# Kernel tuning notes

Measured on AMD Instinct MI355X. Metric: run time of the kernel, lower is better.

Reference implementation:

```python
import jax, jax.numpy as jnp
import numpy as np


def setup_inputs() -> dict:
    key = jax.random.key(0)
    ks = jax.random.split(key, 5)
    B, Cin, Ch, H, W, K = 8, 64, 64, 128, 128, 3
    fan_in = (Cin + Ch) * K * K
    return {
        "x": jax.random.normal(ks[0], (B, Cin, H, W), jnp.float32),
        "prev_h": jax.random.normal(ks[1], (B, Ch, H, W), jnp.float32),
        "prev_c": jax.random.normal(ks[2], (B, Ch, H, W), jnp.float32),
        "W_gates": jax.random.normal(ks[3], (4 * Ch, Cin + Ch, K, K), jnp.float32) / np.sqrt(fan_in),
        "b_gates": jax.random.normal(ks[4], (4 * Ch,), jnp.float32) * 0.01,
    }


def reference(x, prev_h, prev_c, W_gates, b_gates):
    # ConvLSTM cell: conv over concat(input, prev_h) -> 4 gates -> gating.
    pad = W_gates.shape[-1] // 2
    stacked = jnp.concatenate([x, prev_h], axis=1)  # [B, Cin+Ch, H, W]
    gates = jax.lax.conv_general_dilated(
        stacked, W_gates,
        window_strides=(1, 1),
        padding=[(pad, pad), (pad, pad)],
        dimension_numbers=("NCHW", "OIHW", "NCHW"),
    ) + b_gates[None, :, None, None]  # [B, 4*Ch, H, W]
    in_gate, remember_gate, out_gate, cell_gate = jnp.split(gates, 4, axis=1)
    in_gate = jax.nn.sigmoid(in_gate)
    remember_gate = jax.nn.sigmoid(remember_gate)
    out_gate = jax.nn.sigmoid(out_gate)
    cell_gate = jnp.tanh(cell_gate)
    cell = in_gate * cell_gate + remember_gate * prev_c
    hidden = out_gate * jnp.tanh(cell)
    return (hidden, cell)
```

## Files before the change

### kernel.cpp

```cpp
#include <hip/hip_runtime.h>

typedef __attribute__((ext_vector_type(8))) short short8;
typedef __attribute__((ext_vector_type(4))) short short4v;
typedef __attribute__((ext_vector_type(4))) float float4v;

#define NPIX_HID 8388608
#define PST 132

__device__ __forceinline__ short f2bf(float f) {
    union { float f; unsigned u; } v; v.f = f;
    unsigned r = (v.u + 0x7FFFu + ((v.u >> 16) & 1u)) >> 16;
    return (short)r;
}

__device__ __forceinline__ float sigmoidf_(float v) { return 1.f / (1.f + __expf(-v)); }
__device__ __forceinline__ float tanhf_(float v)    { return 2.f / (1.f + __expf(-2.f * v)) - 1.f; }

__global__ void wprep(const float* __restrict__ W, short* __restrict__ A) {
    int tid = blockIdx.x * 256 + threadIdx.x;
    if (tid >= 9 * 16 * 256 * 8) return;
    int j   = tid & 7;
    int co  = (tid >> 3) & 255;
    int cig = (tid >> 11) & 15;
    int kk  = tid >> 15;
    int ci  = cig * 8 + j;
    A[tid] = f2bf(W[co * 1152 + ci * 9 + kk]);
}

__global__ __launch_bounds__(256, 2) void convlstm_main(
    const float* __restrict__ x, const float* __restrict__ ph,
    const float* __restrict__ pc, const short* __restrict__ aprep,
    const float* __restrict__ bg, float* __restrict__ out)
{
    __shared__ short Bs[4 * 66 * PST];

    const int tid  = threadIdx.x;
    const int lane = tid & 63;
    const int wave = tid >> 6;
    const int l15  = lane & 15;
    const int quad = lane >> 4;

    const int t  = blockIdx.x;
    const int x0 = (t & 1) * 64;
    const int y0 = ((t >> 1) & 63) * 2;
    const int b  = t >> 7;

    for (int i = tid; i < 4224; i += 256) {
        const int px  = i % 66;
        const int ro  = i / 66;
        const int oct = ro & 15;
        const int row = ro >> 4;
        const int ysrc = y0 + row - 1;
        const int xsrc = x0 + px - 1;
        short4v lo = {0,0,0,0}, hi = {0,0,0,0};
        if ((unsigned)ysrc < 128u && (unsigned)xsrc < 128u) {
            const float* src = (oct < 8) ? x : ph;
            const float* sp = src + (((b * 64 + (oct & 7) * 8) * 128 + ysrc) * 128 + xsrc);
#pragma unroll
            for (int j = 0; j < 4; ++j) lo[j] = f2bf(sp[j * 16384]);
#pragma unroll
            for (int j = 0; j < 4; ++j) hi[j] = f2bf(sp[(j + 4) * 16384]);
        }
        short* dst = &Bs[(row * 66 + px) * PST + oct * 8];
        *(short4v*)dst       = lo;
        *(short4v*)(dst + 4) = hi;
    }
    __syncthreads();

    float4v acc[4][8];
#pragma unroll
    for (int mt = 0; mt < 4; ++mt)
#pragma unroll
        for (int nt = 0; nt < 8; ++nt)
            acc[mt][nt] = (float4v){0.f, 0.f, 0.f, 0.f};

    const short* ap = aprep + quad * 2048 + (wave * 16 + l15) * 8;
    short8 abuf[2][4];
#pragma unroll
    for (int mt = 0; mt < 4; ++mt) abuf[0][mt] = *(const short8*)(ap + mt * 512);

    const short* bb = &Bs[l15 * PST + quad * 8];

#pragma unroll 1
    for (int ky = 0; ky < 3; ++ky) {
#pragma unroll 1
        for (int kx = 0; kx < 3; ++kx) {
#pragma unroll
            for (int kc = 0; kc < 4; ++kc) {
                const int cur = kc & 1, nxt = cur ^ 1;
                const bool last = (ky == 2) & (kx == 2) & (kc == 3);
                const short* apn = last ? ap : (ap + 8192);
#pragma unroll
                for (int mt = 0; mt < 4; ++mt)
                    abuf[nxt][mt] = *(const short8*)(apn + mt * 512);
                ap = apn;

                short8 bfr[8];
#pragma unroll
                for (int nt = 0; nt < 8; ++nt) {
                    const short* bp = bb + (nt >> 2) * (66 * PST) + (nt & 3) * (16 * PST) + kc * 32;
                    short4v lo = *(const short4v*)bp;
                    short4v hi = *(const short4v*)(bp + 4);
                    bfr[nt] = __builtin_shufflevector(lo, hi, 0, 1, 2, 3, 4, 5, 6, 7);
                }
#pragma unroll
                for (int mt = 0; mt < 4; ++mt)
#pragma unroll
                    for (int nt = 0; nt < 8; ++nt)
                        acc[mt][nt] = __builtin_amdgcn_mfma_f32_16x16x32_bf16(
                            abuf[cur][mt], bfr[nt], acc[mt][nt], 0, 0, 0);
            }
            bb += PST;
        }
        bb += 63 * PST;
    }

#pragma unroll
    for (int nt = 0; nt < 8; ++nt) {
        const int y  = y0 + (nt >> 2);
        const int px = x0 + ((nt & 3) << 4) + l15;
#pragma unroll
        for (int r = 0; r < 4; ++r) {
            const int c = wave * 16 + quad * 4 + r;
            const float gi = acc[0][nt][r] + bg[c];
            const float gf = acc[1][nt][r] + bg[64 + c];
            const float go = acc[2][nt][r] + bg[128 + c];
            const float gc = acc[3][nt][r] + bg[192 + c];
            const float ig = sigmoidf_(gi);
            const float fg = sigmoidf_(gf);
            const float og = sigmoidf_(go);
            const float cg = tanhf_(gc);
            const int idx = ((b * 64 + c) * 128 + y) * 128 + px;
            const float cell = ig * cg + fg * pc[idx];
            const float hid  = og * tanhf_(cell);
            out[idx] = hid;
            out[NPIX_HID + idx] = cell;
        }
    }
}

extern "C" void kernel_launch(void* const* d_in, const int* in_sizes, int n_in,
                              void* d_out, int out_size, void* d_ws, size_t ws_size,
                              hipStream_t stream) {
    const float* x  = (const float*)d_in[0];
    const float* ph = (const float*)d_in[1];
    const float* pc = (const float*)d_in[2];
    const float* W  = (const float*)d_in[3];
    const float* bg = (const float*)d_in[4];
    float* out = (float*)d_out;
    short* aprep = (short*)d_ws;

    wprep<<<1152, 256, 0, stream>>>(W, aprep);
    convlstm_main<<<1024, 256, 0, stream>>>(x, ph, pc, aprep, bg, out);
}
```

Baseline: 219.5 us.

## Halve output tile to one row per block and double-buffer B fragments

Each block now computes a single output row of 64 pixels instead of two rows, which halves the accumulator registers and the LDS halo tile. The launch doubles the grid and asks for three blocks per CU. B-operand fragments are also prefetched one k-chunk ahead into a double buffer, so LDS reads overlap the MFMAs. The cost is less reuse of the halo and weights per block: 3 input rows are staged per output row instead of 4 per two rows, and weight loads per output are doubled.

```diff
diff --git a/kernel.cpp b/kernel.cpp
--- a/kernel.cpp
+++ b/kernel.cpp
@@ -27,12 +27,12 @@
     A[tid] = f2bf(W[co * 1152 + ci * 9 + kk]);
 }
 
-__global__ __launch_bounds__(256, 2) void convlstm_main(
+__global__ __launch_bounds__(256, 3) void convlstm_main(
     const float* __restrict__ x, const float* __restrict__ ph,
     const float* __restrict__ pc, const short* __restrict__ aprep,
     const float* __restrict__ bg, float* __restrict__ out)
 {
-    __shared__ short Bs[4 * 66 * PST];
+    __shared__ short Bs[3 * 66 * PST];
 
     const int tid  = threadIdx.x;
     const int lane = tid & 63;
@@ -42,10 +42,10 @@
 
     const int t  = blockIdx.x;
     const int x0 = (t & 1) * 64;
-    const int y0 = ((t >> 1) & 63) * 2;
-    const int b  = t >> 7;
+    const int y0 = (t >> 1) & 127;
+    const int b  = t >> 8;
 
-    for (int i = tid; i < 4224; i += 256) {
+    for (int i = tid; i < 3168; i += 256) {
         const int px  = i % 66;
         const int ro  = i / 66;
         const int oct = ro & 15;
@@ -67,11 +67,11 @@
     }
     __syncthreads();
 
-    float4v acc[4][8];
+    float4v acc[4][4];
 #pragma unroll
     for (int mt = 0; mt < 4; ++mt)
 #pragma unroll
-        for (int nt = 0; nt < 8; ++nt)
+        for (int nt = 0; nt < 4; ++nt)
             acc[mt][nt] = (float4v){0.f, 0.f, 0.f, 0.f};
 
     const short* ap = aprep + quad * 2048 + (wave * 16 + l15) * 8;
@@ -80,45 +80,56 @@
     for (int mt = 0; mt < 4; ++mt) abuf[0][mt] = *(const short8*)(ap + mt * 512);
 
     const short* bb = &Bs[l15 * PST + quad * 8];
+    short8 bfr[2][4];
+#pragma unroll
+    for (int nt = 0; nt < 4; ++nt) {
+        const short* bp = bb + nt * (16 * PST);
+        short4v lo = *(const short4v*)bp;
+        short4v hi = *(const short4v*)(bp + 4);
+        bfr[0][nt] = __builtin_shufflevector(lo, hi, 0, 1, 2, 3, 4, 5, 6, 7);
+    }
 
 #pragma unroll 1
     for (int ky = 0; ky < 3; ++ky) {
 #pragma unroll 1
         for (int kx = 0; kx < 3; ++kx) {
+            const bool lastkx = (ky == 2) & (kx == 2);
+            const short* bbn = bb + ((kx == 2) ? 64 * PST : PST);
 #pragma unroll
             for (int kc = 0; kc < 4; ++kc) {
                 const int cur = kc & 1, nxt = cur ^ 1;
-                const bool last = (ky == 2) & (kx == 2) & (kc == 3);
+                const bool last = lastkx & (kc == 3);
+
                 const short* apn = last ? ap : (ap + 8192);
 #pragma unroll
                 for (int mt = 0; mt < 4; ++mt)
                     abuf[nxt][mt] = *(const short8*)(apn + mt * 512);
                 ap = apn;
 
-                short8 bfr[8];
+                const short* bq = (kc == 3) ? (lastkx ? bb : bbn) : bb;
+                const int kcn = (kc + 1) & 3;
 #pragma unroll
-                for (int nt = 0; nt < 8; ++nt) {
-                    const short* bp = bb + (nt >> 2) * (66 * PST) + (nt & 3) * (16 * PST) + kc * 32;
+                for (int nt = 0; nt < 4; ++nt) {
+                    const short* bp = bq + nt * (16 * PST) + kcn * 32;
                     short4v lo = *(const short4v*)bp;
                     short4v hi = *(const short4v*)(bp + 4);
-                    bfr[nt] = __builtin_shufflevector(lo, hi, 0, 1, 2, 3, 4, 5, 6, 7);
+                    bfr[nxt][nt] = __builtin_shufflevector(lo, hi, 0, 1, 2, 3, 4, 5, 6, 7);
                 }
+
 #pragma unroll
                 for (int mt = 0; mt < 4; ++mt)
 #pragma unroll
-                    for (int nt = 0; nt < 8; ++nt)
+                    for (int nt = 0; nt < 4; ++nt)
                         acc[mt][nt] = __builtin_amdgcn_mfma_f32_16x16x32_bf16(
-                            abuf[cur][mt], bfr[nt], acc[mt][nt], 0, 0, 0);
+                            abuf[cur][mt], bfr[cur][nt], acc[mt][nt], 0, 0, 0);
             }
-            bb += PST;
+            bb = bbn;
         }
-        bb += 63 * PST;
     }
 
 #pragma unroll
-    for (int nt = 0; nt < 8; ++nt) {
-        const int y  = y0 + (nt >> 2);
-        const int px = x0 + ((nt & 3) << 4) + l15;
+    for (int nt = 0; nt < 4; ++nt) {
+        const int px = x0 + (nt << 4) + l15;
 #pragma unroll
         for (int r = 0; r < 4; ++r) {
             const int c = wave * 16 + quad * 4 + r;
@@ -130,7 +141,7 @@
             const float fg = sigmoidf_(gf);
             const float og = sigmoidf_(go);
             const float cg = tanhf_(gc);
-            const int idx = ((b * 64 + c) * 128 + y) * 128 + px;
+            const int idx = ((b * 64 + c) * 128 + y0) * 128 + px;
             const float cell = ig * cg + fg * pc[idx];
             const float hid  = og * tanhf_(cell);
             out[idx] = hid;
@@ -151,5 +162,5 @@
     short* aprep = (short*)d_ws;
 
     wprep<<<1152, 256, 0, stream>>>(W, aprep);
-    convlstm_main<<<1024, 256, 0, stream>>>(x, ph, pc, aprep, bg, out);
+    convlstm_main<<<2048, 256, 0, stream>>>(x, ph, pc, aprep, bg, out);
 }
```

Measured after the change: 239.9 us. +9.3%, slower.
